# Performance work log

Measured on AMD Instinct MI355X. Metric: run time of the kernel, lower is better.

## Reference

```python
import jax, jax.numpy as jnp
import numpy as np

N, K, D = 65536, 4096, 512
EPS_NORM = 1e-12
EPS_LOG = 1e-10


def _l2norm(x):
    # F.normalize(dim=-1): x / max(||x||, eps)
    n = jnp.sqrt(jnp.sum(x * x, axis=-1, keepdims=True))
    return x / jnp.maximum(n, EPS_NORM)


def setup_inputs() -> dict:
    key = jax.random.key(0)
    k1, k2, k3 = jax.random.split(key, 3)
    z_e = jax.random.normal(k1, (N, D), dtype=jnp.float32)
    embeddings = jax.random.normal(k2, (K, D), dtype=jnp.float32)
    logit_scale = jnp.ones((1,), dtype=jnp.float32) * 10.0
    residual_weight = jnp.asarray(0.3, dtype=jnp.float32)
    return {"z_e": z_e, "embeddings": embeddings,
            "logit_scale": logit_scale, "residual_weight": residual_weight}


def reference(z_e, embeddings, logit_scale, residual_weight):
    # cosine-similarity routing logits: [N, K]
    z_e_norm = _l2norm(z_e)
    emb_norm = _l2norm(embeddings)
    logits = logit_scale * jnp.einsum('nd,kd->nk', z_e_norm, emb_norm)

    # eval path (not training / not kmeans-initialized): hard argmax + gather
    indices = jnp.argmax(logits, axis=-1)          # [N] int
    z_q_pure = embeddings[indices]                 # [N, D]

    # learnable residual blend
    alpha = jax.nn.sigmoid(residual_weight)
    z_q = alpha * z_q_pure + (1.0 - alpha) * z_e

    # codebook usage perplexity
    probs = jax.nn.softmax(logits, axis=-1)        # [N, K]
    avg_probs = jnp.mean(probs, axis=0)            # [K]
    perplexity = jnp.exp(-jnp.sum(avg_probs * jnp.log(avg_probs + EPS_LOG)))

    return (z_q, indices, perplexity, alpha)
```

## Files before the change

### kernel.cpp

```cpp
#include <hip/hip_runtime.h>
#include <cstdint>
#include <cstddef>

#define N_ROWS 65536
#define K_CODES 4096
#define DIM 512
#define ND_OUT ((size_t)N_ROWS * DIM)

typedef __attribute__((ext_vector_type(8))) short  short8v;
typedef __attribute__((ext_vector_type(4))) float  f32x4;

#define WS_PACKED   0u
#define WS_SSUM     524288u
#define WS_AVGP     786432u
#define WS_ARN      802816u
#define WS_BRN      1064960u
#define WS_PLANES   2097152ull
#define SZ_APLANE   67108864ull
#define SZ_BPLANE   4194304ull
#define NEED_B      (WS_PLANES + 2*SZ_APLANE + 2*SZ_BPLANE)

#define PE_AH 0
#define PE_AL 33554432
#define PE_BH 67108864
#define PE_BL 69206016

#define GLOAD_LDS16(gsrc, ldst) \
  __builtin_amdgcn_global_load_lds((const __attribute__((address_space(1))) void*)(gsrc), \
                                   (__attribute__((address_space(3))) void*)(ldst), 16, 0, 0)

__device__ inline unsigned long long pack_max(float v, unsigned idx) {
    unsigned u = __float_as_uint(v);
    u = (u & 0x80000000u) ? ~u : (u | 0x80000000u);
    return ((unsigned long long)u << 32) | (unsigned)(~idx);
}

__device__ inline ushort bf16rn(float f) {
    unsigned u = __float_as_uint(f);
    u += 0x7FFFu + ((u >> 16) & 1u);
    return (ushort)(u >> 16);
}
__device__ inline float bf16f(ushort h) { return __uint_as_float((unsigned)h << 16); }

__global__ __launch_bounds__(256) void norm_split(const float* __restrict__ x,
                                                  ushort* __restrict__ hi,
                                                  ushort* __restrict__ lo,
                                                  float* __restrict__ nrm,
                                                  const float* __restrict__ scale_ptr) {
    int lane = threadIdx.x & 63;
    int row  = blockIdx.x * 4 + (threadIdx.x >> 6);
    const float4* x4 = reinterpret_cast<const float4*>(x) + (size_t)row * (DIM / 4);
    float4 v0 = x4[lane];
    float4 v1 = x4[64 + lane];
    float s = v0.x*v0.x + v0.y*v0.y + v0.z*v0.z + v0.w*v0.w
            + v1.x*v1.x + v1.y*v1.y + v1.z*v1.z + v1.w*v1.w;
#pragma unroll
    for (int off = 32; off; off >>= 1) s += __shfl_xor(s, off);

    ushort4 h0, l0, h1, l1;
    h0.x = bf16rn(v0.x); l0.x = bf16rn(v0.x - bf16f(h0.x));
    h0.y = bf16rn(v0.y); l0.y = bf16rn(v0.y - bf16f(h0.y));
    h0.z = bf16rn(v0.z); l0.z = bf16rn(v0.z - bf16f(h0.z));
    h0.w = bf16rn(v0.w); l0.w = bf16rn(v0.w - bf16f(h0.w));
    h1.x = bf16rn(v1.x); l1.x = bf16rn(v1.x - bf16f(h1.x));
    h1.y = bf16rn(v1.y); l1.y = bf16rn(v1.y - bf16f(h1.y));
    h1.z = bf16rn(v1.z); l1.z = bf16rn(v1.z - bf16f(h1.z));
    h1.w = bf16rn(v1.w); l1.w = bf16rn(v1.w - bf16f(h1.w));
    ushort4* hi4 = reinterpret_cast<ushort4*>(hi) + (size_t)row * (DIM / 4);
    ushort4* lo4 = reinterpret_cast<ushort4*>(lo) + (size_t)row * (DIM / 4);
    hi4[lane] = h0; hi4[64 + lane] = h1;
    lo4[lane] = l0; lo4[64 + lane] = l1;

    if (lane == 0) {
        float scale = scale_ptr ? scale_ptr[0] : 1.0f;
        nrm[row] = scale / fmaxf(sqrtf(s), 1e-12f);
    }
}

template <int EPI, int NREG>
__global__ __launch_bounds__(512, 2) void mfma3(
        const ushort* __restrict__ planes,
        const float* __restrict__ arn, const float* __restrict__ brn,
        unsigned long long* __restrict__ packed, float* __restrict__ ssum,
        float* __restrict__ avgp) {
    constexpr int NSTEPS = NREG * 16;
    __shared__ __align__(16) char lds[131072];

    const int tid  = threadIdx.x;
    const int lane = tid & 63;
    const int wavei = __builtin_amdgcn_readfirstlane(tid >> 6);
    const int wr = wavei >> 1, wc = wavei & 1;
    const int r16 = lane & 15, kg = lane >> 4;

    const int orig = blockIdx.x;
    const int swz  = (orig & 7) * 512 + (orig >> 3);
    const int row0 = (swz >> 4) * 256, col0 = (swz & 15) * 256;

    size_t rowoff[4];
    int ldso[4];
    bool uA[4];
#pragma unroll
    for (int j = 0; j < 4; ++j) {
        int u = wavei * 4 + j;
        bool a = (u < 16);
        int g0 = a ? row0 : col0;
        rowoff[j] = (size_t)(g0 + (u & 15) * 16 + r16) * DIM + kg * 8;
        ldso[j] = u * 1024;
        uA[j] = a;
    }

    auto STAGE = [&](int ks, char* slot) {
        int rg  = (ks >> 4) & 3;
        int kk  = (ks & 15) * 32;
        int bA = (rg & 1) ? PE_AL : PE_AH;
        int bB = ((rg ^ (rg >> 1)) & 1) ? PE_BL : PE_BH;
#pragma unroll
        for (int j = 0; j < 4; ++j) {
            const ushort* src = planes + (uA[j] ? bA : bB) + kk + rowoff[j];
            GLOAD_LDS16(src, slot + ldso[j]);
        }
    };

    f32x4 acc[4][8];
#pragma unroll
    for (int m = 0; m < 4; ++m)
#pragma unroll
        for (int n = 0; n < 8; ++n) acc[m][n] = f32x4{0.f, 0.f, 0.f, 0.f};

    char* const S0 = lds;
    char* const S1 = lds + 32768;
    char* const S2 = lds + 65536;
    char* const S3 = lds + 98304;

#define KSTEP(CUR, NXT, KS, DO_STAGE, VMC)                                              \
    do {                                                                                \
        short8v a_[4], b_[8];                                                           \
        _Pragma("unroll")                                                               \
        for (int m = 0; m < 4; ++m)                                                     \
            a_[m] = *(const short8v*)((CUR) + (wr * 4 + m) * 1024 + lane * 16);         \
        _Pragma("unroll")                                                               \
        for (int n = 0; n < 8; ++n)                                                     \
            b_[n] = *(const short8v*)((CUR) + 16384 + (wc * 8 + n) * 1024 + lane * 16); \
        asm volatile("s_waitcnt lgkmcnt(0)" ::: "memory");                              \
        if (DO_STAGE) STAGE((KS), (NXT));                                               \
        asm volatile("s_waitcnt vmcnt(" #VMC ")" ::: "memory");                         \
        asm volatile("s_barrier" ::: "memory");                                         \
        __builtin_amdgcn_sched_barrier(0);                                              \
        __builtin_amdgcn_s_setprio(1);                                                  \
        _Pragma("unroll")                                                               \
        for (int m = 0; m < 4; ++m)                                                     \
            _Pragma("unroll")                                                           \
            for (int n = 0; n < 8; ++n)                                                 \
                acc[m][n] = __builtin_amdgcn_mfma_f32_16x16x32_bf16(a_[m], b_[n],       \
                                                                    acc[m][n], 0, 0, 0);\
        __builtin_amdgcn_s_setprio(0);                                                  \
        __builtin_amdgcn_sched_barrier(0);                                              \
    } while (0)

    STAGE(0, S0);
    STAGE(1, S1);
    asm volatile("s_waitcnt vmcnt(4)" ::: "memory");
    asm volatile("s_barrier" ::: "memory");
    __builtin_amdgcn_sched_barrier(0);

#pragma unroll 1
    for (int kt0 = 0; kt0 < NSTEPS - 4; kt0 += 4) {
        KSTEP(S0, S2, kt0 + 2, true, 4);
        KSTEP(S1, S3, kt0 + 3, true, 4);
        KSTEP(S2, S0, kt0 + 4, true, 4);
        KSTEP(S3, S1, kt0 + 5, true, 4);
    }
    KSTEP(S0, S2, NSTEPS - 2, true, 4);
    KSTEP(S1, S3, NSTEPS - 1, true, 4);
    KSTEP(S2, S0, 0, false, 0);
    KSTEP(S3, S0, 0, false, 0);
#undef KSTEP

    const int g = lane >> 4, c15 = lane & 15;
    float bc[8];
#pragma unroll
    for (int n = 0; n < 8; ++n) bc[n] = brn[col0 + wc * 128 + n * 16 + c15];

    if constexpr (EPI == 0) {
#pragma unroll
        for (int m = 0; m < 4; ++m)
#pragma unroll
            for (int rr = 0; rr < 4; ++rr) {
                const int grow = row0 + wr * 64 + m * 16 + g * 4 + rr;
                const float ar = arn[grow];
                float mx = -1e30f; int mi = 0; float se = 0.f;
#pragma unroll
                for (int n = 0; n < 8; ++n) {
                    float lg = acc[m][n][rr] * ar * bc[n];
                    int gcol = col0 + wc * 128 + n * 16 + c15;
                    se += __expf(lg);
                    if (lg > mx || (lg == mx && gcol < mi)) { mx = lg; mi = gcol; }
                }
#pragma unroll
                for (int off = 1; off < 16; off <<= 1) {
                    float om = __shfl_xor(mx, off, 16);
                    int   oi = __shfl_xor(mi, off, 16);
                    float os = __shfl_xor(se, off, 16);
                    se += os;
                    if (om > mx || (om == mx && oi < mi)) { mx = om; mi = oi; }
                }
                if (c15 == 0) {
                    atomicMax(packed + grow, pack_max(mx, (unsigned)mi));
                    atomicAdd(&ssum[grow], se);
                }
            }
    } else {
        float cp[8] = {0.f, 0.f, 0.f, 0.f, 0.f, 0.f, 0.f, 0.f};
#pragma unroll
        for (int m = 0; m < 4; ++m)
#pragma unroll
            for (int rr = 0; rr < 4; ++rr) {
                const int grow = row0 + wr * 64 + m * 16 + g * 4 + rr;
                const float ar = arn[grow];
                const float si = 1.0f / ssum[grow];
#pragma unroll
                for (int n = 0; n < 8; ++n)
                    cp[n] += __expf(acc[m][n][rr] * ar * bc[n]) * si;
            }
#pragma unroll
        for (int n = 0; n < 8; ++n) {
            cp[n] += __shfl_xor(cp[n], 16);
            cp[n] += __shfl_xor(cp[n], 32);
        }
        float* sm = (float*)lds;
        if (g == 0) {
#pragma unroll
            for (int n = 0; n < 8; ++n) sm[wavei * 128 + n * 16 + c15] = cp[n];
        }
        __syncthreads();
        if (tid < 256) {
            int wcc = tid >> 7, j = tid & 127;
            float s = sm[(0 + wcc) * 128 + j] + sm[(2 + wcc) * 128 + j]
                    + sm[(4 + wcc) * 128 + j] + sm[(6 + wcc) * 128 + j];
            atomicAdd(&avgp[col0 + wcc * 128 + j], s);
        }
    }
}

template <int PASS>
__global__ __launch_bounds__(256) void gemm_pass(
        const float* __restrict__ A, const float* __restrict__ B,
        const float* __restrict__ arn, const float* __restrict__ brn,
        unsigned long long* __restrict__ packed, float* __restrict__ ssum,
        float* __restrict__ avgp) {
    __shared__ __align__(16) float As[16][132];
    __shared__ __align__(16) float Bs[16][132];
    const int tid = threadIdx.x;
    const int tr = tid >> 4, tc = tid & 15;
    const int row0 = blockIdx.y * 128, col0 = blockIdx.x * 128;

    float acc[8][8] = {};
    const float4* A4 = reinterpret_cast<const float4*>(A);
    const float4* B4 = reinterpret_cast<const float4*>(B);

    for (int d0 = 0; d0 < DIM; d0 += 16) {
#pragma unroll
        for (int l = 0; l < 2; ++l) {
            int q = tid + l * 256;
            int r = q >> 2, dq = q & 3;
            float4 av = A4[(size_t)(row0 + r) * (DIM / 4) + (d0 >> 2) + dq];
            float4 bv = B4[(size_t)(col0 + r) * (DIM / 4) + (d0 >> 2) + dq];
            As[dq*4+0][r] = av.x; As[dq*4+1][r] = av.y; As[dq*4+2][r] = av.z; As[dq*4+3][r] = av.w;
            Bs[dq*4+0][r] = bv.x; Bs[dq*4+1][r] = bv.y; Bs[dq*4+2][r] = bv.z; Bs[dq*4+3][r] = bv.w;
        }
        __syncthreads();
#pragma unroll
        for (int dd = 0; dd < 16; ++dd) {
            float4 a0 = *reinterpret_cast<const float4*>(&As[dd][tr * 4]);
            float4 a1 = *reinterpret_cast<const float4*>(&As[dd][64 + tr * 4]);
            float4 b0 = *reinterpret_cast<const float4*>(&Bs[dd][tc * 4]);
            float4 b1 = *reinterpret_cast<const float4*>(&Bs[dd][64 + tc * 4]);
            float av[8] = {a0.x, a0.y, a0.z, a0.w, a1.x, a1.y, a1.z, a1.w};
            float bv[8] = {b0.x, b0.y, b0.z, b0.w, b1.x, b1.y, b1.z, b1.w};
#pragma unroll
            for (int i = 0; i < 8; ++i)
#pragma unroll
                for (int j = 0; j < 8; ++j)
                    acc[i][j] = fmaf(av[i], bv[j], acc[i][j]);
        }
        __syncthreads();
    }

    int rows[8], cols[8];
    float ar[8], bcv[8];
#pragma unroll
    for (int i = 0; i < 8; ++i) {
        rows[i] = (i < 4) ? (tr * 4 + i) : (64 + tr * 4 + i - 4);
        ar[i] = arn[row0 + rows[i]];
    }
#pragma unroll
    for (int j = 0; j < 8; ++j) {
        cols[j] = (j < 4) ? (tc * 4 + j) : (64 + tc * 4 + j - 4);
        bcv[j] = brn[col0 + cols[j]];
    }

    if constexpr (PASS == 1) {
#pragma unroll
        for (int i = 0; i < 8; ++i) {
            float m = -1e30f; int mi = 0; float se = 0.0f;
#pragma unroll
            for (int j = 0; j < 8; ++j) {
                float l = acc[i][j] * ar[i] * bcv[j];
                int c = col0 + cols[j];
                if (l > m || (l == m && c < mi)) { m = l; mi = c; }
                se += expf(l);
            }
#pragma unroll
            for (int off = 1; off < 16; off <<= 1) {
                float om = __shfl_xor(m, off, 16);
                int   oi = __shfl_xor(mi, off, 16);
                float os = __shfl_xor(se, off, 16);
                se += os;
                if (om > m || (om == m && oi < mi)) { m = om; mi = oi; }
            }
            if (tc == 0) {
                int grow = row0 + rows[i];
                atomicMax(packed + grow, pack_max(m, (unsigned)mi));
                atomicAdd(&ssum[grow], se);
            }
        }
    } else {
        float sinv[8];
#pragma unroll
        for (int i = 0; i < 8; ++i) sinv[i] = 1.0f / ssum[row0 + rows[i]];
        float cp[8] = {};
#pragma unroll
        for (int i = 0; i < 8; ++i)
#pragma unroll
            for (int j = 0; j < 8; ++j)
                cp[j] += expf(acc[i][j] * ar[i] * bcv[j]) * sinv[i];
        __syncthreads();
        float* red = &As[0][0];
#pragma unroll
        for (int j = 0; j < 8; ++j) red[tr * 128 + cols[j]] = cp[j];
        __syncthreads();
        if (tid < 128) {
            float s = 0.0f;
#pragma unroll
            for (int t = 0; t < 16; ++t) s += red[t * 128 + tid];
            atomicAdd(&avgp[col0 + tid], s);
        }
    }
}

__global__ __launch_bounds__(256) void zq_kernel(const float* __restrict__ ze,
                                                 const float* __restrict__ emb,
                                                 const unsigned long long* __restrict__ packed,
                                                 const float* __restrict__ resw,
                                                 float* __restrict__ out) {
    int q = blockIdx.x * 256 + threadIdx.x;
    int n = q >> 7, d4 = q & 127;
    unsigned idx = ~(unsigned)(packed[n] & 0xFFFFFFFFull);
    float alpha = 1.0f / (1.0f + expf(-resw[0]));
    float4 e = reinterpret_cast<const float4*>(emb)[(size_t)idx * 128 + d4];
    float4 z = reinterpret_cast<const float4*>(ze)[(size_t)n * 128 + d4];
    float4 o;
    o.x = alpha * e.x + (1.0f - alpha) * z.x;
    o.y = alpha * e.y + (1.0f - alpha) * z.y;
    o.z = alpha * e.z + (1.0f - alpha) * z.z;
    o.w = alpha * e.w + (1.0f - alpha) * z.w;
    reinterpret_cast<float4*>(out)[(size_t)n * 128 + d4] = o;
    if (d4 == 0) out[ND_OUT + n] = (float)idx;
}

__global__ __launch_bounds__(256) void finalize_kernel(const float* __restrict__ avgp,
                                                       const float* __restrict__ resw,
                                                       float* __restrict__ out) {
    float acc = 0.0f;
    for (int k = threadIdx.x; k < K_CODES; k += 256) {
        float p = avgp[k] * (1.0f / (float)N_ROWS);
        acc += p * logf(p + 1e-10f);
    }
    __shared__ float red[4];
#pragma unroll
    for (int off = 32; off; off >>= 1) acc += __shfl_xor(acc, off);
    int lane = threadIdx.x & 63, wave = threadIdx.x >> 6;
    if (lane == 0) red[wave] = acc;
    __syncthreads();
    if (threadIdx.x == 0) {
        float s = red[0] + red[1] + red[2] + red[3];
        out[ND_OUT + N_ROWS]     = expf(-s);
        out[ND_OUT + N_ROWS + 1] = 1.0f / (1.0f + expf(-resw[0]));
    }
}

extern "C" void kernel_launch(void* const* d_in, const int* in_sizes, int n_in,
                              void* d_out, int out_size, void* d_ws, size_t ws_size,
                              hipStream_t stream) {
    const float* ze   = (const float*)d_in[0];
    const float* emb  = (const float*)d_in[1];
    const float* ls   = (const float*)d_in[2];
    const float* resw = (const float*)d_in[3];
    float* out = (float*)d_out;

    char* ws = (char*)d_ws;
    unsigned long long* packed = (unsigned long long*)(ws + WS_PACKED);
    float* ssum = (float*)(ws + WS_SSUM);
    float* avgp = (float*)(ws + WS_AVGP);
    float* arn  = (float*)(ws + WS_ARN);
    float* brn  = (float*)(ws + WS_BRN);

    hipMemsetAsync(d_ws, 0, 802816, stream);

    if (ws_size >= NEED_B) {
        ushort* planes = (ushort*)(ws + WS_PLANES);
        norm_split<<<N_ROWS / 4, 256, 0, stream>>>(ze, planes + PE_AH, planes + PE_AL, arn, ls);
        norm_split<<<K_CODES / 4, 256, 0, stream>>>(emb, planes + PE_BH, planes + PE_BL, brn, nullptr);

        mfma3<0, 4><<<4096, 512, 0, stream>>>(planes, arn, brn, packed, ssum, avgp);
        mfma3<2, 1><<<4096, 512, 0, stream>>>(planes, arn, brn, packed, ssum, avgp);
    } else {
        float* arn2 = arn; float* brn2 = brn;
        {
        }
        extern __global__ void rownorm_only(const float*, float*, const float*);
        rownorm_only<<<N_ROWS / 4, 256, 0, stream>>>(ze, arn2, ls);
        rownorm_only<<<K_CODES / 4, 256, 0, stream>>>(emb, brn2, nullptr);
        dim3 grid(K_CODES / 128, N_ROWS / 128);
        gemm_pass<1><<<grid, 256, 0, stream>>>(ze, emb, arn2, brn2, packed, ssum, avgp);
        gemm_pass<2><<<grid, 256, 0, stream>>>(ze, emb, arn2, brn2, packed, ssum, avgp);
    }

    zq_kernel<<<(N_ROWS * (DIM / 4)) / 256, 256, 0, stream>>>(ze, emb, packed, resw, out);
    finalize_kernel<<<1, 256, 0, stream>>>(avgp, resw, out);
}

__global__ __launch_bounds__(256) void rownorm_only(const float* __restrict__ x,
                                                    float* __restrict__ outp,
                                                    const float* __restrict__ scale_ptr) {
    int lane = threadIdx.x & 63;
    int row  = blockIdx.x * 4 + (threadIdx.x >> 6);
    const float4* x4 = reinterpret_cast<const float4*>(x) + (size_t)row * (DIM / 4);
    float4 v0 = x4[lane];
    float4 v1 = x4[64 + lane];
    float s = v0.x*v0.x + v0.y*v0.y + v0.z*v0.z + v0.w*v0.w
            + v1.x*v1.x + v1.y*v1.y + v1.z*v1.z + v1.w*v1.w;
#pragma unroll
    for (int off = 32; off; off >>= 1) s += __shfl_xor(s, off);
    if (lane == 0) {
        float scale = scale_ptr ? scale_ptr[0] : 1.0f;
        outp[row] = scale / fmaxf(sqrtf(s), 1e-12f);
    }
}
```

Before: 1.730 ms.

## Add hand-scheduled split-bf16 MFMA kernel with 4-buffer LDS pipeline for pass one

Replaces the first-pass GEMM (argmax plus row exp-sum) with a new kernel, mfma4. It stages the hi and lo bf16 planes into four rotating 32KB LDS regions using direct global-to-LDS loads. It orders the hi*hi, hi*lo, lo*hi and lo*lo MFMA groups with explicit waitcnt, barriers and setprio, so loads for the next k-step overlap compute. The epilogue does the argmax and sum-of-exp reduction with 16-lane shuffles and atomics, using the fast __expf. The fallback path's rownorm_only declaration is also moved and cleaned up. The risk is subtle hazards from the manual vmcnt counts and barriers, and small numeric differences from __expf.

```diff
diff --git a/kernel.cpp b/kernel.cpp
--- a/kernel.cpp
+++ b/kernel.cpp
@@ -75,6 +75,157 @@
         float scale = scale_ptr ? scale_ptr[0] : 1.0f;
         nrm[row] = scale / fmaxf(sqrtf(s), 1e-12f);
     }
+}
+
+__global__ __launch_bounds__(512, 2) void mfma4(
+        const ushort* __restrict__ planes,
+        const float* __restrict__ arn, const float* __restrict__ brn,
+        unsigned long long* __restrict__ packed, float* __restrict__ ssum) {
+    __shared__ __align__(16) char lds[131072];
+    char* const R0 = lds;
+    char* const R1 = lds + 32768;
+    char* const R2 = lds + 65536;
+    char* const R3 = lds + 98304;
+
+    const int tid  = threadIdx.x;
+    const int lane = tid & 63;
+    const int wavei = __builtin_amdgcn_readfirstlane(tid >> 6);
+    const int wr = wavei >> 1, wc = wavei & 1;
+    const int r16 = lane & 15, kg = lane >> 4;
+
+    const int orig = blockIdx.x;
+    const int swz  = (orig & 7) * 512 + (orig >> 3);
+    const int row0 = (swz >> 4) * 256, col0 = (swz & 15) * 256;
+
+    size_t rowoff[4];
+    int ldso[4];
+    bool uA[4];
+#pragma unroll
+    for (int j = 0; j < 4; ++j) {
+        int u = wavei * 4 + j;
+        bool a = (u < 16);
+        int g0 = a ? row0 : col0;
+        rowoff[j] = (size_t)(g0 + (u & 15) * 16 + r16) * DIM + kg * 8;
+        ldso[j] = u * 1024;
+        uA[j] = a;
+    }
+
+#define STAGE_HI(KK, DST)                                                              \
+    { _Pragma("unroll")                                                                \
+      for (int j = 0; j < 4; ++j)                                                      \
+          GLOAD_LDS16(planes + (uA[j] ? PE_AH : PE_BH) + rowoff[j] + (KK),             \
+                      (DST) + ldso[j]); }
+#define STAGE_LO(KK, DST)                                                              \
+    { _Pragma("unroll")                                                                \
+      for (int j = 0; j < 4; ++j)                                                      \
+          GLOAD_LDS16(planes + (uA[j] ? PE_AL : PE_BL) + rowoff[j] + (KK),             \
+                      (DST) + ldso[j]); }
+
+    f32x4 acc[4][8];
+#pragma unroll
+    for (int m = 0; m < 4; ++m)
+#pragma unroll
+        for (int n = 0; n < 8; ++n) acc[m][n] = f32x4{0.f, 0.f, 0.f, 0.f};
+
+#define MFMA32(AV, BV)                                                                 \
+    _Pragma("unroll")                                                                  \
+    for (int m_ = 0; m_ < 4; ++m_)                                                     \
+        _Pragma("unroll")                                                              \
+        for (int n_ = 0; n_ < 8; ++n_)                                                 \
+            acc[m_][n_] = __builtin_amdgcn_mfma_f32_16x16x32_bf16((AV)[m_], (BV)[n_],  \
+                                                                  acc[m_][n_], 0, 0, 0);
+
+#define STEP(HI, LO, HI2, LO2, KNEXT, DOSTAGE, VM2)                                    \
+    {                                                                                  \
+        short8v ah_[4], bh_[8], bl_[8], al_[4];                                        \
+                    \
+        asm volatile("s_waitcnt vmcnt(4)" ::: "memory");                               \
+        asm volatile("s_barrier" ::: "memory");                                        \
+        __builtin_amdgcn_sched_barrier(0);                                             \
+        _Pragma("unroll")                                                              \
+        for (int m = 0; m < 4; ++m)                                                    \
+            ah_[m] = *(const short8v*)((HI) + (wr * 4 + m) * 1024 + lane * 16);        \
+        _Pragma("unroll")                                                              \
+        for (int n = 0; n < 8; ++n)                                                    \
+            bh_[n] = *(const short8v*)((HI) + 16384 + (wc * 8 + n) * 1024 + lane * 16);\
+        if (DOSTAGE) STAGE_HI((KNEXT) * 32, HI2);                                      \
+        asm volatile("s_waitcnt lgkmcnt(0)" ::: "memory");                             \
+        __builtin_amdgcn_sched_barrier(0);                                             \
+        __builtin_amdgcn_s_setprio(1);                                                 \
+        MFMA32(ah_, bh_);                                                              \
+        __builtin_amdgcn_s_setprio(0);                                                 \
+                                      \
+        asm volatile("s_waitcnt vmcnt(" #VM2 ")" ::: "memory");                        \
+        asm volatile("s_barrier" ::: "memory");                                        \
+        __builtin_amdgcn_sched_barrier(0);                                             \
+        _Pragma("unroll")                                                              \
+        for (int n = 0; n < 8; ++n)                                                    \
+            bl_[n] = *(const short8v*)((LO) + 16384 + (wc * 8 + n) * 1024 + lane * 16);\
+        asm volatile("s_waitcnt lgkmcnt(0)" ::: "memory");                             \
+        __builtin_amdgcn_sched_barrier(0);                                             \
+        __builtin_amdgcn_s_setprio(1);                                                 \
+        MFMA32(ah_, bl_);                                                              \
+        __builtin_amdgcn_s_setprio(0);                                                 \
+                               \
+        _Pragma("unroll")                                                              \
+        for (int m = 0; m < 4; ++m)                                                    \
+            al_[m] = *(const short8v*)((LO) + (wr * 4 + m) * 1024 + lane * 16);        \
+        if (DOSTAGE) STAGE_LO((KNEXT) * 32, LO2);                                      \
+        asm volatile("s_waitcnt lgkmcnt(0)" ::: "memory");                             \
+        __builtin_amdgcn_sched_barrier(0);                                             \
+        __builtin_amdgcn_s_setprio(1);                                                 \
+        MFMA32(al_, bh_);                                                              \
+        MFMA32(al_, bl_);                                                              \
+        __builtin_amdgcn_s_setprio(0);                                                 \
+    }
+
+    STAGE_HI(0, R0);
+    STAGE_LO(0, R1);
+
+#pragma unroll 1
+    for (int t = 0; t < 14; t += 2) {
+        STEP(R0, R1, R2, R3, t + 1, 1, 4);
+        STEP(R2, R3, R0, R1, t + 2, 1, 4);
+    }
+    STEP(R0, R1, R2, R3, 15, 1, 4);
+    STEP(R2, R3, R0, R1, 0, 0, 0);
+#undef STEP
+#undef MFMA32
+#undef STAGE_HI
+#undef STAGE_LO
+
+    const int g = lane >> 4, c15 = lane & 15;
+    float bc[8];
+#pragma unroll
+    for (int n = 0; n < 8; ++n) bc[n] = brn[col0 + wc * 128 + n * 16 + c15];
+
+#pragma unroll
+    for (int m = 0; m < 4; ++m)
+#pragma unroll
+        for (int rr = 0; rr < 4; ++rr) {
+            const int grow = row0 + wr * 64 + m * 16 + g * 4 + rr;
+            const float ar = arn[grow];
+            float mx = -1e30f; int mi = 0; float se = 0.f;
+#pragma unroll
+            for (int n = 0; n < 8; ++n) {
+                float lg = acc[m][n][rr] * ar * bc[n];
+                int gcol = col0 + wc * 128 + n * 16 + c15;
+                se += __expf(lg);
+                if (lg > mx || (lg == mx && gcol < mi)) { mx = lg; mi = gcol; }
+            }
+#pragma unroll
+            for (int off = 1; off < 16; off <<= 1) {
+                float om = __shfl_xor(mx, off, 16);
+                int   oi = __shfl_xor(mi, off, 16);
+                float os = __shfl_xor(se, off, 16);
+                se += os;
+                if (om > mx || (om == mx && oi < mi)) { mx = om; mi = oi; }
+            }
+            if (c15 == 0) {
+                atomicMax(packed + grow, pack_max(mx, (unsigned)mi));
+                atomicAdd(&ssum[grow], se);
+            }
+        }
 }
 
 template <int EPI, int NREG>
@@ -348,6 +499,24 @@
     }
 }
 
+__global__ __launch_bounds__(256) void rownorm_only(const float* __restrict__ x,
+                                                    float* __restrict__ outp,
+                                                    const float* __restrict__ scale_ptr) {
+    int lane = threadIdx.x & 63;
+    int row  = blockIdx.x * 4 + (threadIdx.x >> 6);
+    const float4* x4 = reinterpret_cast<const float4*>(x) + (size_t)row * (DIM / 4);
+    float4 v0 = x4[lane];
+    float4 v1 = x4[64 + lane];
+    float s = v0.x*v0.x + v0.y*v0.y + v0.z*v0.z + v0.w*v0.w
+            + v1.x*v1.x + v1.y*v1.y + v1.z*v1.z + v1.w*v1.w;
+#pragma unroll
+    for (int off = 32; off; off >>= 1) s += __shfl_xor(s, off);
+    if (lane == 0) {
+        float scale = scale_ptr ? scale_ptr[0] : 1.0f;
+        outp[row] = scale / fmaxf(sqrtf(s), 1e-12f);
+    }
+}
+
 __global__ __launch_bounds__(256) void zq_kernel(const float* __restrict__ ze,
                                                  const float* __restrict__ emb,
                                                  const unsigned long long* __restrict__ packed,
@@ -412,38 +581,16 @@
         norm_split<<<N_ROWS / 4, 256, 0, stream>>>(ze, planes + PE_AH, planes + PE_AL, arn, ls);
         norm_split<<<K_CODES / 4, 256, 0, stream>>>(emb, planes + PE_BH, planes + PE_BL, brn, nullptr);
 
-        mfma3<0, 4><<<4096, 512, 0, stream>>>(planes, arn, brn, packed, ssum, avgp);
+        mfma4<<<4096, 512, 0, stream>>>(planes, arn, brn, packed, ssum);
         mfma3<2, 1><<<4096, 512, 0, stream>>>(planes, arn, brn, packed, ssum, avgp);
     } else {
-        float* arn2 = arn; float* brn2 = brn;
-        {
-        }
-        extern __global__ void rownorm_only(const float*, float*, const float*);
-        rownorm_only<<<N_ROWS / 4, 256, 0, stream>>>(ze, arn2, ls);
-        rownorm_only<<<K_CODES / 4, 256, 0, stream>>>(emb, brn2, nullptr);
+        rownorm_only<<<N_ROWS / 4, 256, 0, stream>>>(ze, arn, ls);
+        rownorm_only<<<K_CODES / 4, 256, 0, stream>>>(emb, brn, nullptr);
         dim3 grid(K_CODES / 128, N_ROWS / 128);
-        gemm_pass<1><<<grid, 256, 0, stream>>>(ze, emb, arn2, brn2, packed, ssum, avgp);
-        gemm_pass<2><<<grid, 256, 0, stream>>>(ze, emb, arn2, brn2, packed, ssum, avgp);
+        gemm_pass<1><<<grid, 256, 0, stream>>>(ze, emb, arn, brn, packed, ssum, avgp);
+        gemm_pass<2><<<grid, 256, 0, stream>>>(ze, emb, arn, brn, packed, ssum, avgp);
     }
 
     zq_kernel<<<(N_ROWS * (DIM / 4)) / 256, 256, 0, stream>>>(ze, emb, packed, resw, out);
     finalize_kernel<<<1, 256, 0, stream>>>(avgp, resw, out);
 }
-
-__global__ __launch_bounds__(256) void rownorm_only(const float* __restrict__ x,
-                                                    float* __restrict__ outp,
-                                                    const float* __restrict__ scale_ptr) {
-    int lane = threadIdx.x & 63;
-    int row  = blockIdx.x * 4 + (threadIdx.x >> 6);
-    const float4* x4 = reinterpret_cast<const float4*>(x) + (size_t)row * (DIM / 4);
-    float4 v0 = x4[lane];
-    float4 v1 = x4[64 + lane];
-    float s = v0.x*v0.x + v0.y*v0.y + v0.z*v0.z + v0.w*v0.w
-            + v1.x*v1.x + v1.y*v1.y + v1.z*v1.z + v1.w*v1.w;
-#pragma unroll
-    for (int off = 32; off; off >>= 1) s += __shfl_xor(s, off);
-    if (lane == 0) {
-        float scale = scale_ptr ? scale_ptr[0] : 1.0f;
-        outp[row] = scale / fmaxf(sqrtf(s), 1e-12f);
-    }
-}
```

Result: faster. 1.471 ms, median of 2 (-15.0%).
